# Kernel tuning notes

Hardware: AMD Instinct MI355X
Metric: run time of the kernel (lower is better)

The kernel has to match this reference:

```python
import jax, jax.numpy as jnp
import numpy as np
import math

NEG = -1000000.0


def setup_inputs() -> dict:
    key = jax.random.key(0)
    ks = jax.random.split(key, 8)
    B, S, D = 4, 2048, 1024
    std = 1.0 / math.sqrt(D)
    return {
        "queries": jax.random.normal(ks[0], (B, S, D), jnp.float32),
        "keys": jax.random.normal(ks[1], (B, S, D), jnp.float32),
        "values": jax.random.normal(ks[2], (B, S, D), jnp.float32),
        "valid_len": jax.random.randint(ks[3], (B,), 1, S, dtype=jnp.int64 if jax.config.jax_enable_x64 else jnp.int32),
        "W_q": jax.random.normal(ks[4], (D, D), jnp.float32) * std,
        "W_k": jax.random.normal(ks[5], (D, D), jnp.float32) * std,
        "W_v": jax.random.normal(ks[6], (D, D), jnp.float32) * std,
        "W_o": jax.random.normal(ks[7], (D, D), jnp.float32) * std,
    }


def reference(queries, keys, values, valid_len, W_q, W_k, W_v, W_o):
    NUM_HEADS = 16
    B, S, D = queries.shape
    hd = D // NUM_HEADS

    def split_heads(x):
        # (B, S, D) -> (B, H, S, hd)
        return x.reshape(B, -1, NUM_HEADS, hd).transpose(0, 2, 1, 3)

    # nn.Linear with weight W applies x @ W.T
    q = split_heads(queries @ W_q.T)
    k = split_heads(keys @ W_k.T)
    v = split_heads(values @ W_v.T)

    scale = 1.0 / math.sqrt(hd)
    scores = jnp.einsum('bhqd,bhkd->bhqk', q, k) * scale  # (B, H, Sq, Sk)

    # key-padding mask from valid_len: positions >= valid_len are masked
    kpos = jnp.arange(scores.shape[-1])
    pad_mask = kpos[None, None, None, :] >= valid_len[:, None, None, None]
    scores = jnp.where(pad_mask, NEG, scores)
    attn = jax.nn.softmax(scores, axis=-1)

    out = jnp.einsum('bhqk,bhkd->bhqd', attn, v)  # (B, H, Sq, hd)
    out = out.transpose(0, 2, 1, 3).reshape(B, -1, D)
    return out @ W_o.T
```

## Files before the change

kernel.cpp:

```cpp
#include <hip/hip_runtime.h>
#include <hip/hip_bf16.h>

using bf16_t = __bf16;
using bf16x8 = __attribute__((ext_vector_type(8))) __bf16;
using bf16x4 = __attribute__((ext_vector_type(4))) __bf16;
using bf16x2 = __attribute__((ext_vector_type(2))) __bf16;
using f32x4  = __attribute__((ext_vector_type(4))) float;

#define S_  2048
#define D_  1024

typedef __attribute__((address_space(1))) unsigned int glb_u32;
typedef __attribute__((address_space(3))) unsigned int lds_u32;

__device__ __forceinline__ void async_cp16(const void* g, void* lds) {
    __builtin_amdgcn_global_load_lds(
        (glb_u32*)(unsigned long long)g,
        (lds_u32*)(unsigned int)(unsigned long long)lds,
        16, 0, 0);
}

__global__ __launch_bounds__(256) void cast_f32_bf16(const float* __restrict__ s,
                                                     bf16_t* __restrict__ d, int n4) {
    int i = blockIdx.x * 256 + threadIdx.x;
    if (i >= n4) return;
    float4 f = reinterpret_cast<const float4*>(s)[i];
    bf16x4 o;
    o[0] = (bf16_t)f.x; o[1] = (bf16_t)f.y; o[2] = (bf16_t)f.z; o[3] = (bf16_t)f.w;
    reinterpret_cast<bf16x4*>(d)[i] = o;
}

__global__ __launch_bounds__(256) void cast2_f32_bf16(const float* __restrict__ a, const float* __restrict__ b,
                                                      bf16_t* __restrict__ oa, bf16_t* __restrict__ ob, int n4) {
    int i = blockIdx.x * 256 + threadIdx.x;
    if (i >= n4) return;
    const float* s = blockIdx.y ? b : a;
    bf16_t*      d = blockIdx.y ? ob : oa;
    float4 f = reinterpret_cast<const float4*>(s)[i];
    bf16x4 o;
    o[0] = (bf16_t)f.x; o[1] = (bf16_t)f.y; o[2] = (bf16_t)f.z; o[3] = (bf16_t)f.w;
    reinterpret_cast<bf16x4*>(d)[i] = o;
}

__global__ __launch_bounds__(256) void cast4_f32_bf16(const float* __restrict__ a, const float* __restrict__ b,
                                                      const float* __restrict__ c, const float* __restrict__ dd,
                                                      bf16_t* __restrict__ oa, bf16_t* __restrict__ ob,
                                                      bf16_t* __restrict__ oc, bf16_t* __restrict__ od, int n4) {
    int i = blockIdx.x * 256 + threadIdx.x;
    if (i >= n4) return;
    const float* s; bf16_t* d;
    int w = blockIdx.y;
    if      (w == 0) { s = a;  d = oa; }
    else if (w == 1) { s = b;  d = ob; }
    else if (w == 2) { s = c;  d = oc; }
    else             { s = dd; d = od; }
    float4 f = reinterpret_cast<const float4*>(s)[i];
    bf16x4 o;
    o[0] = (bf16_t)f.x; o[1] = (bf16_t)f.y; o[2] = (bf16_t)f.z; o[3] = (bf16_t)f.w;
    reinterpret_cast<bf16x4*>(d)[i] = o;
}

template <int OUTMODE>
__global__ __launch_bounds__(256) void gemm_bt(const bf16_t* __restrict__ A,
                                               const bf16_t* __restrict__ Bt,
                                               void* __restrict__ Cv, float scale) {
    __shared__ bf16_t As[128 * 32];
    __shared__ bf16_t Bs[128 * 32];
    const int K = 1024;
    int tid  = threadIdx.x;
    int lane = tid & 63;
    int w    = tid >> 6;
    int l15  = lane & 15, quad = lane >> 4;
    int m0 = blockIdx.y * 128, n0 = blockIdx.x * 128;
    int wm = (w >> 1) * 64, wn = (w & 1) * 64;

    const bf16_t* Ag = A  + (size_t)(m0 + (tid >> 2)) * K + (tid & 3) * 8;
    const bf16_t* Bg = Bt + (size_t)(n0 + (tid >> 2)) * K + (tid & 3) * 8;
    bf16_t* Asw = As + tid * 8;
    bf16_t* Bsw = Bs + tid * 8;

    f32x4 acc[4][4] = {};

    for (int k0 = 0; k0 < K; k0 += 32) {
        __syncthreads();
        async_cp16(Ag + k0,                    Asw);
        async_cp16(Ag + k0 + (size_t)64 * K,   Asw + 2048);
        async_cp16(Bg + k0,                    Bsw);
        async_cp16(Bg + k0 + (size_t)64 * K,   Bsw + 2048);
        __syncthreads();
        bf16x8 af[4], bfr[4];
#pragma unroll
        for (int t = 0; t < 4; t++) {
            af[t]  = *reinterpret_cast<const bf16x8*>(&As[(wm + t * 16 + l15) * 32 + quad * 8]);
            bfr[t] = *reinterpret_cast<const bf16x8*>(&Bs[(wn + t * 16 + l15) * 32 + quad * 8]);
        }
#pragma unroll
        for (int mt = 0; mt < 4; mt++)
#pragma unroll
            for (int nt = 0; nt < 4; nt++)
                acc[mt][nt] = __builtin_amdgcn_mfma_f32_16x16x32_bf16(af[mt], bfr[nt], acc[mt][nt], 0, 0, 0);
    }

#pragma unroll
    for (int mt = 0; mt < 4; mt++)
#pragma unroll
        for (int nt = 0; nt < 4; nt++) {
            if (OUTMODE == 2) {
                int m = m0 + wm + mt * 16 + quad * 4;
                int n = n0 + wn + nt * 16 + l15;
                bf16x4 o4;
#pragma unroll
                for (int r = 0; r < 4; r++) o4[r] = (bf16_t)(acc[mt][nt][r] * scale);
                size_t vrow = (size_t)((m >> 11) * 16 + (n >> 6)) * 64 + (n & 63);
                *reinterpret_cast<bf16x4*>(&((bf16_t*)Cv)[vrow * S_ + (m & 2047)]) = o4;
            } else {
#pragma unroll
                for (int r = 0; r < 4; r++) {
                    int m = m0 + wm + mt * 16 + quad * 4 + r;
                    int n = n0 + wn + nt * 16 + l15;
                    size_t idx = (size_t)m * 1024 + n;
                    if (OUTMODE == 1) reinterpret_cast<float*>(Cv)[idx] = acc[mt][nt][r] * scale;
                    else              reinterpret_cast<bf16_t*>(Cv)[idx] = (bf16_t)(acc[mt][nt][r] * scale);
                }
            }
        }
}

__global__ __launch_bounds__(256) void attn_fused(const bf16_t* __restrict__ Qp,
                                                  const bf16_t* __restrict__ Kp,
                                                  const bf16_t* __restrict__ Vt,
                                                  const int* __restrict__ vlen_p,
                                                  bf16_t* __restrict__ Out) {
    __shared__ bf16_t Qs[2 * 128 * 32];
    __shared__ bf16_t Ks[2 * 64 * 32];
    __shared__ bf16_t Vs[64 * 68];

    int tid  = threadIdx.x;
    int lane = tid & 63, w = tid >> 6;
    int l15  = lane & 15, quad = lane >> 4;
    int qblk = blockIdx.x;
    int bh = blockIdx.y, b = bh >> 4, h = bh & 15;
    int vlen = vlen_p[b];
    int nkb  = (vlen + 63) >> 6;

    const bf16_t* Qg = Qp + (size_t)(b * S_ + qblk * 128) * D_ + h * 64;
    const bf16_t* Kg = Kp + (size_t)b * S_ * D_ + h * 64;
    const bf16_t* Vg = Vt + (size_t)bh * 64 * S_;

#pragma unroll
    for (int j = 0; j < 4; j++) {
        int linear = j * 256 + tid;
        int kk = linear >> 9, row = (linear >> 2) & 127, sub = linear & 3;
        async_cp16(Qg + (size_t)row * D_ + kk * 32 + sub * 8, Qs + linear * 8);
    }
    __syncthreads();
    bf16x8 qf[2][2];
#pragma unroll
    for (int qt = 0; qt < 2; qt++)
#pragma unroll
        for (int kk = 0; kk < 2; kk++)
            qf[qt][kk] = *reinterpret_cast<const bf16x8*>(&Qs[kk * 4096 + (w * 32 + qt * 16 + l15) * 32 + quad * 8]);

    f32x4 o[2][4] = {};
    float l_st[2] = {0.f, 0.f};

    for (int kb = 0; kb < nkb; kb++) {
        __syncthreads();
#pragma unroll
        for (int j = 0; j < 2; j++) {
            int linear = j * 256 + tid;
            int kk = linear >> 8, row = (linear >> 2) & 63, sub = linear & 3;
            async_cp16(Kg + (size_t)(kb * 64 + row) * D_ + kk * 32 + sub * 8, Ks + linear * 8);
        }
#pragma unroll
        for (int j = 0; j < 2; j++) {
            int linear = j * 256 + tid;
            int row = linear >> 3, c8 = linear & 7;
            uint4 vv = *reinterpret_cast<const uint4*>(&Vg[(size_t)row * S_ + kb * 64 + c8 * 8]);
            uint2* vp = reinterpret_cast<uint2*>(&Vs[row * 68 + c8 * 8]);
            vp[0] = make_uint2(vv.x, vv.y);
            vp[1] = make_uint2(vv.z, vv.w);
        }
        __syncthreads();

        f32x4 sc[2][4] = {};
#pragma unroll
        for (int nt = 0; nt < 4; nt++)
#pragma unroll
            for (int kk = 0; kk < 2; kk++) {
                bf16x8 kf = *reinterpret_cast<const bf16x8*>(&Ks[kk * 2048 + (nt * 16 + l15) * 32 + quad * 8]);
                sc[0][nt] = __builtin_amdgcn_mfma_f32_16x16x32_bf16(kf, qf[0][kk], sc[0][nt], 0, 0, 0);
                sc[1][nt] = __builtin_amdgcn_mfma_f32_16x16x32_bf16(kf, qf[1][kk], sc[1][nt], 0, 0, 0);
            }

        bool partial = (vlen & 63) && (kb == nkb - 1);
        bf16x8 pf[2][2];
        if (!partial) {
#pragma unroll
            for (int qt = 0; qt < 2; qt++) {
                float lacc = 0.f;
#pragma unroll
                for (int nt = 0; nt < 4; nt++)
#pragma unroll
                    for (int r = 0; r < 4; r++) {
                        float p = __builtin_exp2f(sc[qt][nt][r]);
                        lacc += p;
                        pf[qt][nt >> 1][(nt & 1) * 4 + r] = (bf16_t)p;
                    }
                l_st[qt] += lacc;
            }
        } else {
#pragma unroll
            for (int qt = 0; qt < 2; qt++) {
                float lacc = 0.f;
#pragma unroll
                for (int nt = 0; nt < 4; nt++)
#pragma unroll
                    for (int r = 0; r < 4; r++) {
                        float p = __builtin_exp2f(sc[qt][nt][r]);
                        if (kb * 64 + nt * 16 + quad * 4 + r >= vlen) p = 0.f;
                        lacc += p;
                        pf[qt][nt >> 1][(nt & 1) * 4 + r] = (bf16_t)p;
                    }
                l_st[qt] += lacc;
            }
        }

#pragma unroll
        for (int np = 0; np < 2; np++)
#pragma unroll
            for (int dt = 0; dt < 4; dt++) {
                bf16x4 v0 = *reinterpret_cast<const bf16x4*>(&Vs[(dt * 16 + l15) * 68 + np * 32 + quad * 4]);
                bf16x4 v1 = *reinterpret_cast<const bf16x4*>(&Vs[(dt * 16 + l15) * 68 + np * 32 + 16 + quad * 4]);
                bf16x8 vf;
#pragma unroll
                for (int j = 0; j < 4; j++) { vf[j] = v0[j]; vf[4 + j] = v1[j]; }
                o[0][dt] = __builtin_amdgcn_mfma_f32_16x16x32_bf16(vf, pf[0][np], o[0][dt], 0, 0, 0);
                o[1][dt] = __builtin_amdgcn_mfma_f32_16x16x32_bf16(vf, pf[1][np], o[1][dt], 0, 0, 0);
            }
    }

    float inv[2];
#pragma unroll
    for (int qt = 0; qt < 2; qt++) {
        float l = l_st[qt];
        l += __shfl_xor(l, 16);
        l += __shfl_xor(l, 32);
        inv[qt] = 1.0f / l;
    }

    __syncthreads();
    bf16_t* T = Qs;
#pragma unroll
    for (int qt = 0; qt < 2; qt++) {
        int row = w * 32 + qt * 16 + l15;
#pragma unroll
        for (int dt = 0; dt < 4; dt++) {
            int phys = ((dt * 2 + (quad >> 1)) ^ (l15 & 7));
            int base = row * 64 + phys * 8 + (quad & 1) * 4;
            bf16x2 t0, t1;
            t0[0] = (bf16_t)(o[qt][dt][0] * inv[qt]);
            t0[1] = (bf16_t)(o[qt][dt][1] * inv[qt]);
            t1[0] = (bf16_t)(o[qt][dt][2] * inv[qt]);
            t1[1] = (bf16_t)(o[qt][dt][3] * inv[qt]);
            *reinterpret_cast<bf16x2*>(&T[base])     = t0;
            *reinterpret_cast<bf16x2*>(&T[base + 2]) = t1;
        }
    }
    __syncthreads();
    {
        int row = w * 32 + (lane >> 1);
        int ch  = lane & 1;
        size_t orow = ((size_t)(b * S_ + qblk * 128) + row) * D_ + h * 64 + ch * 32;
#pragma unroll
        for (int k = 0; k < 4; k++) {
            int phys = (ch * 4 + k) ^ (row & 7);
            bf16x8 frag = *reinterpret_cast<const bf16x8*>(&T[row * 64 + phys * 8]);
            *reinterpret_cast<bf16x8*>(&Out[orow + k * 8]) = frag;
        }
    }
}

extern "C" void kernel_launch(void* const* d_in, const int* in_sizes, int n_in,
                              void* d_out, int out_size, void* d_ws, size_t ws_size,
                              hipStream_t stream) {
    const float* q  = (const float*)d_in[0];
    const float* k  = (const float*)d_in[1];
    const float* v  = (const float*)d_in[2];
    const int*   vl = (const int*)d_in[3];
    const float* Wq = (const float*)d_in[4];
    const float* Wk = (const float*)d_in[5];
    const float* Wv = (const float*)d_in[6];
    const float* Wo = (const float*)d_in[7];
    float* out = (float*)d_out;

    bf16_t* ws = (bf16_t*)d_ws;
    const size_t SD = (size_t)8192 * 1024;
    const size_t WW = (size_t)1024 * 1024;
    bf16_t* tmpA = ws;
    bf16_t* tmpB = ws + SD;
    bf16_t* Qp   = ws + 2 * SD;
    bf16_t* Kp   = ws + 3 * SD;
    bf16_t* Vt   = ws + 4 * SD;
    bf16_t* Wqb  = ws + 5 * SD;
    bf16_t* Wkb  = Wqb + WW;
    bf16_t* Wvb  = Wqb + 2 * WW;
    bf16_t* Wob  = Wqb + 3 * WW;

    const float cs = 0.18033688f;
    dim3 blk(256);
    dim3 gg(8, 64);

    cast4_f32_bf16<<<dim3(1024, 4), blk, 0, stream>>>(Wq, Wk, Wv, Wo, Wqb, Wkb, Wvb, Wob, 262144);
    cast2_f32_bf16<<<dim3(8192, 2), blk, 0, stream>>>(q, k, tmpA, tmpB, 2097152);

    gemm_bt<0><<<gg, blk, 0, stream>>>(tmpA, Wqb, Qp, cs);
    gemm_bt<0><<<gg, blk, 0, stream>>>(tmpB, Wkb, Kp, 1.0f);
    cast_f32_bf16<<<dim3(8192), blk, 0, stream>>>(v, tmpA, 2097152);
    gemm_bt<2><<<gg, blk, 0, stream>>>(tmpA, Wvb, Vt, 1.0f);

    attn_fused<<<dim3(16, 64), blk, 0, stream>>>(Qp, Kp, Vt, vl, tmpB);
    gemm_bt<1><<<gg, blk, 0, stream>>>(tmpB, Wob, out, 1.0f);
}
```

Baseline: 366.1 us.

## Restructure attention kernel: double-buffered async K/V, 64-row Q tiles, load-balanced block order

Rewrites the fused attention kernel. Each block now covers 64 query rows instead of 128, and K and V are double-buffered in XOR-swizzled shared memory using async global-to-LDS copies, so the next tile loads while the current one computes. Blocks use a 1D grid ordered by batch from longest to shortest valid length, which balances load. The cost is twice the blocks and half the Q reuse per K/V tile, so K/V global traffic doubles.

New measurement: 355.5 us. -2.9%, faster.

```diff
diff --git a/kernel.cpp b/kernel.cpp
--- a/kernel.cpp
+++ b/kernel.cpp
@@ -131,153 +131,147 @@
                                                   const bf16_t* __restrict__ Vt,
                                                   const int* __restrict__ vlen_p,
                                                   bf16_t* __restrict__ Out) {
-    __shared__ bf16_t Qs[2 * 128 * 32];
-    __shared__ bf16_t Ks[2 * 64 * 32];
-    __shared__ bf16_t Vs[64 * 68];
+    __shared__ bf16_t smem[4][64 * 64];
 
     int tid  = threadIdx.x;
     int lane = tid & 63, w = tid >> 6;
     int l15  = lane & 15, quad = lane >> 4;
-    int qblk = blockIdx.x;
-    int bh = blockIdx.y, b = bh >> 4, h = bh & 15;
+
+    int nk[4], ord[4] = {0, 1, 2, 3};
+#pragma unroll
+    for (int i = 0; i < 4; i++) nk[i] = (vlen_p[i] + 63) >> 6;
+#pragma unroll
+    for (int i = 0; i < 3; i++)
+#pragma unroll
+        for (int j = 0; j < 3 - i; j++)
+            if (nk[ord[j + 1]] > nk[ord[j]]) { int t = ord[j]; ord[j] = ord[j + 1]; ord[j + 1] = t; }
+
+    int bid  = blockIdx.x;
+    int b    = ord[bid >> 9];
+    int t    = bid & 511;
+    int h    = (t & 7) * 2 + ((t >> 3) & 1);
+    int qblk = t >> 4;
     int vlen = vlen_p[b];
     int nkb  = (vlen + 63) >> 6;
 
-    const bf16_t* Qg = Qp + (size_t)(b * S_ + qblk * 128) * D_ + h * 64;
+    const bf16_t* Qg = Qp + (size_t)(b * S_ + qblk * 64) * D_ + h * 64;
     const bf16_t* Kg = Kp + (size_t)b * S_ * D_ + h * 64;
-    const bf16_t* Vg = Vt + (size_t)bh * 64 * S_;
-
-#pragma unroll
-    for (int j = 0; j < 4; j++) {
-        int linear = j * 256 + tid;
-        int kk = linear >> 9, row = (linear >> 2) & 127, sub = linear & 3;
-        async_cp16(Qg + (size_t)row * D_ + kk * 32 + sub * 8, Qs + linear * 8);
-    }
-    __syncthreads();
-    bf16x8 qf[2][2];
-#pragma unroll
-    for (int qt = 0; qt < 2; qt++)
-#pragma unroll
-        for (int kk = 0; kk < 2; kk++)
-            qf[qt][kk] = *reinterpret_cast<const bf16x8*>(&Qs[kk * 4096 + (w * 32 + qt * 16 + l15) * 32 + quad * 8]);
-
-    f32x4 o[2][4] = {};
-    float l_st[2] = {0.f, 0.f};
-
-    for (int kb = 0; kb < nkb; kb++) {
-        __syncthreads();
+    const bf16_t* Vg = Vt + (size_t)(b * 16 + h) * 64 * S_;
+
+    auto stage = [&](const bf16_t* g, size_t rstride, bf16_t* lds) {
 #pragma unroll
         for (int j = 0; j < 2; j++) {
             int linear = j * 256 + tid;
-            int kk = linear >> 8, row = (linear >> 2) & 63, sub = linear & 3;
-            async_cp16(Kg + (size_t)(kb * 64 + row) * D_ + kk * 32 + sub * 8, Ks + linear * 8);
-        }
-#pragma unroll
-        for (int j = 0; j < 2; j++) {
-            int linear = j * 256 + tid;
-            int row = linear >> 3, c8 = linear & 7;
-            uint4 vv = *reinterpret_cast<const uint4*>(&Vg[(size_t)row * S_ + kb * 64 + c8 * 8]);
-            uint2* vp = reinterpret_cast<uint2*>(&Vs[row * 68 + c8 * 8]);
-            vp[0] = make_uint2(vv.x, vv.y);
-            vp[1] = make_uint2(vv.z, vv.w);
-        }
+            int row = linear >> 3, s = linear & 7;
+            async_cp16(g + (size_t)row * rstride + (s ^ (row & 7)) * 8, lds + linear * 8);
+        }
+    };
+
+    stage(Qg, D_, smem[2]);
+    stage(Kg, D_, smem[0]);
+    stage(Vg, S_, smem[1]);
+    __syncthreads();
+
+    bf16x8 qf[2];
+    {
+        int row = w * 16 + l15, x = row & 7;
+#pragma unroll
+        for (int kk = 0; kk < 2; kk++)
+            qf[kk] = *reinterpret_cast<const bf16x8*>(&smem[2][row * 64 + ((kk * 4 + quad) ^ x) * 8]);
+    }
+    __syncthreads();
+
+    f32x4 o[4] = {};
+    float l_st = 0.f;
+
+    for (int kb = 0; kb < nkb; kb++) {
+        int cur = kb & 1;
+        if (kb + 1 < nkb) {
+            int nxt = cur ^ 1;
+            stage(Kg + (size_t)(kb + 1) * 64 * D_, D_, smem[nxt * 2]);
+            stage(Vg + (kb + 1) * 64,              S_, smem[nxt * 2 + 1]);
+        }
+        const bf16_t* Kc = smem[cur * 2];
+        const bf16_t* Vc = smem[cur * 2 + 1];
+
+        f32x4 sc[4] = {};
+#pragma unroll
+        for (int nt = 0; nt < 4; nt++) {
+            int row = nt * 16 + l15, x = row & 7;
+#pragma unroll
+            for (int kk = 0; kk < 2; kk++) {
+                bf16x8 kf = *reinterpret_cast<const bf16x8*>(&Kc[row * 64 + ((kk * 4 + quad) ^ x) * 8]);
+                sc[nt] = __builtin_amdgcn_mfma_f32_16x16x32_bf16(kf, qf[kk], sc[nt], 0, 0, 0);
+            }
+        }
+
+        bool partial = (vlen & 63) && (kb == nkb - 1);
+        bf16x8 pf[2];
+        float lacc = 0.f;
+        if (!partial) {
+#pragma unroll
+            for (int nt = 0; nt < 4; nt++)
+#pragma unroll
+                for (int r = 0; r < 4; r++) {
+                    float p = __builtin_exp2f(sc[nt][r]);
+                    lacc += p;
+                    pf[nt >> 1][(nt & 1) * 4 + r] = (bf16_t)p;
+                }
+        } else {
+#pragma unroll
+            for (int nt = 0; nt < 4; nt++)
+#pragma unroll
+                for (int r = 0; r < 4; r++) {
+                    float p = __builtin_exp2f(sc[nt][r]);
+                    if (kb * 64 + nt * 16 + quad * 4 + r >= vlen) p = 0.f;
+                    lacc += p;
+                    pf[nt >> 1][(nt & 1) * 4 + r] = (bf16_t)p;
+                }
+        }
+        l_st += lacc;
+
+#pragma unroll
+        for (int np = 0; np < 2; np++)
+#pragma unroll
+            for (int dt = 0; dt < 4; dt++) {
+                int row = dt * 16 + l15, x = row & 7;
+                int off = (quad & 1) * 4;
+                bf16x4 v0 = *reinterpret_cast<const bf16x4*>(&Vc[row * 64 + (((np * 4)     + (quad >> 1)) ^ x) * 8 + off]);
+                bf16x4 v1 = *reinterpret_cast<const bf16x4*>(&Vc[row * 64 + (((np * 4 + 2) + (quad >> 1)) ^ x) * 8 + off]);
+                bf16x8 vf;
+#pragma unroll
+                for (int j = 0; j < 4; j++) { vf[j] = v0[j]; vf[4 + j] = v1[j]; }
+                o[dt] = __builtin_amdgcn_mfma_f32_16x16x32_bf16(vf, pf[np], o[dt], 0, 0, 0);
+            }
+
         __syncthreads();
-
-        f32x4 sc[2][4] = {};
-#pragma unroll
-        for (int nt = 0; nt < 4; nt++)
-#pragma unroll
-            for (int kk = 0; kk < 2; kk++) {
-                bf16x8 kf = *reinterpret_cast<const bf16x8*>(&Ks[kk * 2048 + (nt * 16 + l15) * 32 + quad * 8]);
-                sc[0][nt] = __builtin_amdgcn_mfma_f32_16x16x32_bf16(kf, qf[0][kk], sc[0][nt], 0, 0, 0);
-                sc[1][nt] = __builtin_amdgcn_mfma_f32_16x16x32_bf16(kf, qf[1][kk], sc[1][nt], 0, 0, 0);
-            }
-
-        bool partial = (vlen & 63) && (kb == nkb - 1);
-        bf16x8 pf[2][2];
-        if (!partial) {
-#pragma unroll
-            for (int qt = 0; qt < 2; qt++) {
-                float lacc = 0.f;
-#pragma unroll
-                for (int nt = 0; nt < 4; nt++)
-#pragma unroll
-                    for (int r = 0; r < 4; r++) {
-                        float p = __builtin_exp2f(sc[qt][nt][r]);
-                        lacc += p;
-                        pf[qt][nt >> 1][(nt & 1) * 4 + r] = (bf16_t)p;
-                    }
-                l_st[qt] += lacc;
-            }
-        } else {
-#pragma unroll
-            for (int qt = 0; qt < 2; qt++) {
-                float lacc = 0.f;
-#pragma unroll
-                for (int nt = 0; nt < 4; nt++)
-#pragma unroll
-                    for (int r = 0; r < 4; r++) {
-                        float p = __builtin_exp2f(sc[qt][nt][r]);
-                        if (kb * 64 + nt * 16 + quad * 4 + r >= vlen) p = 0.f;
-                        lacc += p;
-                        pf[qt][nt >> 1][(nt & 1) * 4 + r] = (bf16_t)p;
-                    }
-                l_st[qt] += lacc;
-            }
-        }
-
-#pragma unroll
-        for (int np = 0; np < 2; np++)
-#pragma unroll
-            for (int dt = 0; dt < 4; dt++) {
-                bf16x4 v0 = *reinterpret_cast<const bf16x4*>(&Vs[(dt * 16 + l15) * 68 + np * 32 + quad * 4]);
-                bf16x4 v1 = *reinterpret_cast<const bf16x4*>(&Vs[(dt * 16 + l15) * 68 + np * 32 + 16 + quad * 4]);
-                bf16x8 vf;
-#pragma unroll
-                for (int j = 0; j < 4; j++) { vf[j] = v0[j]; vf[4 + j] = v1[j]; }
-                o[0][dt] = __builtin_amdgcn_mfma_f32_16x16x32_bf16(vf, pf[0][np], o[0][dt], 0, 0, 0);
-                o[1][dt] = __builtin_amdgcn_mfma_f32_16x16x32_bf16(vf, pf[1][np], o[1][dt], 0, 0, 0);
-            }
-    }
-
-    float inv[2];
-#pragma unroll
-    for (int qt = 0; qt < 2; qt++) {
-        float l = l_st[qt];
-        l += __shfl_xor(l, 16);
-        l += __shfl_xor(l, 32);
-        inv[qt] = 1.0f / l;
-    }
-
-    __syncthreads();
-    bf16_t* T = Qs;
-#pragma unroll
-    for (int qt = 0; qt < 2; qt++) {
-        int row = w * 32 + qt * 16 + l15;
+    }
+
+    float l = l_st;
+    l += __shfl_xor(l, 16);
+    l += __shfl_xor(l, 32);
+    float inv = 1.0f / l;
+
+    bf16_t* T = smem[0];
+    {
+        int row = w * 16 + l15, x = row & 7;
 #pragma unroll
         for (int dt = 0; dt < 4; dt++) {
-            int phys = ((dt * 2 + (quad >> 1)) ^ (l15 & 7));
-            int base = row * 64 + phys * 8 + (quad & 1) * 4;
-            bf16x2 t0, t1;
-            t0[0] = (bf16_t)(o[qt][dt][0] * inv[qt]);
-            t0[1] = (bf16_t)(o[qt][dt][1] * inv[qt]);
-            t1[0] = (bf16_t)(o[qt][dt][2] * inv[qt]);
-            t1[1] = (bf16_t)(o[qt][dt][3] * inv[qt]);
-            *reinterpret_cast<bf16x2*>(&T[base])     = t0;
-            *reinterpret_cast<bf16x2*>(&T[base + 2]) = t1;
+            bf16x4 o4;
+#pragma unroll
+            for (int r = 0; r < 4; r++) o4[r] = (bf16_t)(o[dt][r] * inv);
+            int slot = dt * 2 + (quad >> 1);
+            *reinterpret_cast<bf16x4*>(&T[row * 64 + (slot ^ x) * 8 + (quad & 1) * 4]) = o4;
         }
     }
     __syncthreads();
     {
-        int row = w * 32 + (lane >> 1);
-        int ch  = lane & 1;
-        size_t orow = ((size_t)(b * S_ + qblk * 128) + row) * D_ + h * 64 + ch * 32;
-#pragma unroll
-        for (int k = 0; k < 4; k++) {
-            int phys = (ch * 4 + k) ^ (row & 7);
-            bf16x8 frag = *reinterpret_cast<const bf16x8*>(&T[row * 64 + phys * 8]);
-            *reinterpret_cast<bf16x8*>(&Out[orow + k * 8]) = frag;
-        }
+        int row = tid >> 2, ch = tid & 3, x = row & 7;
+        size_t obase = (size_t)(b * S_ + qblk * 64 + row) * D_ + h * 64 + ch * 16;
+        bf16x8 f0 = *reinterpret_cast<const bf16x8*>(&T[row * 64 + ((ch * 2)     ^ x) * 8]);
+        bf16x8 f1 = *reinterpret_cast<const bf16x8*>(&T[row * 64 + ((ch * 2 + 1) ^ x) * 8]);
+        *reinterpret_cast<bf16x8*>(&Out[obase])     = f0;
+        *reinterpret_cast<bf16x8*>(&Out[obase + 8]) = f1;
     }
 }
 
@@ -319,6 +313,6 @@
     cast_f32_bf16<<<dim3(8192), blk, 0, stream>>>(v, tmpA, 2097152);
     gemm_bt<2><<<gg, blk, 0, stream>>>(tmpA, Wvb, Vt, 1.0f);
 
-    attn_fused<<<dim3(16, 64), blk, 0, stream>>>(Qp, Kp, Vt, vl, tmpB);
+    attn_fused<<<dim3(2048), blk, 0, stream>>>(Qp, Kp, Vt, vl, tmpB);
     gemm_bt<1><<<gg, blk, 0, stream>>>(tmpB, Wob, out, 1.0f);
 }
```
